# Optimization experiments

Hardware: AMD Instinct MI355X
Metric: run time of the kernel (lower is better)

Reference implementation:

```python
import jax, jax.numpy as jnp
import numpy as np

N_NODES = 8192
N_EDGES = 524288
IN_DIM = 256
HID1 = 128
HID2 = 64


def setup_inputs() -> dict:
    key = jax.random.key(0)
    ks = jax.random.split(key, 10)
    s = 0.05
    x = jax.random.normal(ks[0], (N_NODES, IN_DIM), dtype=jnp.float32)
    edge_index = jax.random.randint(ks[1], (2, N_EDGES), 0, N_NODES, dtype=jnp.int64)
    W1 = jax.random.normal(ks[2], (IN_DIM, HID1), dtype=jnp.float32) * s
    b1 = jnp.zeros((HID1,), dtype=jnp.float32)
    W2 = jax.random.normal(ks[3], (IN_DIM, HID1), dtype=jnp.float32) * s
    b2 = jnp.zeros((HID1,), dtype=jnp.float32)
    Wmu = jax.random.normal(ks[4], (2 * HID1, HID2), dtype=jnp.float32) * s
    bmu = jnp.zeros((HID2,), dtype=jnp.float32)
    Wlv = jax.random.normal(ks[5], (2 * HID1, HID2), dtype=jnp.float32) * s
    blv = jnp.zeros((HID2,), dtype=jnp.float32)
    return {"x": x, "edge_index": edge_index, "W1": W1, "b1": b1,
            "W2": W2, "b2": b2, "Wmu": Wmu, "bmu": bmu, "Wlv": Wlv, "blv": blv}


def _gcn(x, W, b, row, col, norm, n):
    # linear transform, edge-indexed gather, degree-normalized scale, scatter-add
    h = x @ W                                   # [N, out]
    msg = h[col] * norm[:, None]                # [E+N, out]
    agg = jax.ops.segment_sum(msg, row, num_segments=n)
    return agg + b


def reference(x, edge_index, W1, b1, W2, b2, Wmu, bmu, Wlv, blv):
    n = x.shape[0]
    loop = jnp.arange(n, dtype=edge_index.dtype)
    row = jnp.concatenate([edge_index[0], loop])   # add self-loops (GCNConv default)
    col = jnp.concatenate([edge_index[1], loop])
    deg = jax.ops.segment_sum(jnp.ones_like(row, dtype=x.dtype), row, num_segments=n)
    dinv = jnp.where(deg > 0, jax.lax.rsqrt(deg), 0.0)
    norm = dinv[row] * dinv[col]                   # symmetric D^-1/2 A_hat D^-1/2

    h1 = _gcn(x, W1, b1, row, col, norm, n)
    h2 = _gcn(x, W2, b2, row, col, norm, n)
    hc = jnp.concatenate([h1, h2], axis=1)         # [N, 2*HID1]
    mu = _gcn(hc, Wmu, bmu, row, col, norm, n)
    logvar = _gcn(hc, Wlv, blv, row, col, norm, n)
    z = mu                                         # eval-mode reparametrize -> mu
    adj = jax.nn.sigmoid(z @ z.T)                  # InnerProductDecoder.forward_all
    return adj, mu, logvar
```

## Files before the change

### kernel.cpp

```cpp
#include <hip/hip_runtime.h>
#include <hip/hip_bf16.h>

#define N_NODES 8192
#define N_EDGES 524288
#define TOT_EDGES (N_EDGES + N_NODES)
#define IN_DIM 256
#define HID1 128
#define HID2 64
#define DC 128
#define CAP 192
#define FILL_BLK 520

typedef __attribute__((ext_vector_type(8))) short bf16x8;
typedef __attribute__((ext_vector_type(4))) float f32x4;
typedef __attribute__((ext_vector_type(4))) int   i32x4;
typedef __attribute__((ext_vector_type(4))) unsigned short u16x4;

__device__ __forceinline__ float b2f(unsigned short u){
    unsigned int v = ((unsigned int)u) << 16;
    float f; __builtin_memcpy(&f, &v, 4); return f;
}
__device__ __forceinline__ unsigned short f2b(float f){
    __hip_bfloat16 h = __float2bfloat16(f);
    return *(unsigned short*)&h;
}


__global__ __launch_bounds__(256) void k_pre(const float* __restrict__ W1, const float* __restrict__ W2,
                                             const float* __restrict__ Wmu, const float* __restrict__ Wlv,
                                             const float* __restrict__ b1, const float* __restrict__ b2,
                                             unsigned short* __restrict__ WcT, float* __restrict__ cvec,
                                             float* __restrict__ zbase){
    int b = blockIdx.x, t = threadIdx.x;
    if (b < 8){
        ((f32x4*)zbase)[b*256 + t] = (f32x4){0.f,0.f,0.f,0.f};
    } else {
        int r = (b - 8)*2 + (t >> 7);
        int j = t & 127;
        const float* Wsel = (j < 64) ? Wmu : Wlv;
        int jj = j & 63;
        float acc = 0.f;
        for (int k=0;k<HID1;k++){
            acc += W1[r*HID1+k] * Wsel[k*HID2+jj] + W2[r*HID1+k] * Wsel[(HID1+k)*HID2+jj];
        }
        WcT[(size_t)j*IN_DIM + r] = f2b(acc);
        if (r == 0){
            float c = 0.f;
            for (int k=0;k<HID1;k++){
                c += b1[k]*Wsel[k*HID2+jj] + b2[k]*Wsel[(HID1+k)*HID2+jj];
            }
            cvec[j] = c;
        }
    }
}


__global__ __launch_bounds__(256) void k_fill_gemm(const int* __restrict__ ei, int* __restrict__ fillc,
                                                   unsigned short* __restrict__ slots,
                                                   const float* __restrict__ x,
                                                   const unsigned short* __restrict__ WcT,
                                                   unsigned short* __restrict__ Ubf){
    int b = blockIdx.x, t = threadIdx.x;
    if (b < FILL_BLK){
        int e4 = (b*256 + t)*4;
        if (e4 >= TOT_EDGES) return;
        if (e4 < N_EDGES){
            i32x4 rr = *(const i32x4*)(ei + e4);
            i32x4 cc = *(const i32x4*)(ei + N_EDGES + e4);
            #pragma unroll
            for (int j=0;j<4;j++){
                int s = atomicAdd(&fillc[rr[j]], 1);
                if (s < CAP) slots[(size_t)rr[j]*CAP + s] = (unsigned short)cc[j];
            }
        } else {
            #pragma unroll
            for (int j=0;j<4;j++){
                int r = e4 - N_EDGES + j;
                int s = atomicAdd(&fillc[r], 1);
                if (s < CAP) slots[(size_t)r*CAP + s] = (unsigned short)r;
            }
        }
    } else {
        int l  = t & 63;
        int w  = t >> 6;
        int Ibase = (b - FILL_BLK)*32;
        int Jbase = w*32;
        int lr = l & 15;
        int kg = l >> 4;
        f32x4 acc[2][2];
        #pragma unroll
        for (int mt=0;mt<2;mt++)
            #pragma unroll
            for (int nt=0;nt<2;nt++) acc[mt][nt] = (f32x4){0.f,0.f,0.f,0.f};
        #pragma unroll
        for (int kc=0; kc<IN_DIM/32; kc++){
            bf16x8 a[2], bb[2];
            #pragma unroll
            for (int mt=0;mt<2;mt++){
                const float* xr = x + (size_t)(Ibase+mt*16+lr)*IN_DIM + kc*32 + kg*8;
                f32x4 v0 = *(const f32x4*)xr;
                f32x4 v1 = *(const f32x4*)(xr + 4);
                #pragma unroll
                for (int j=0;j<4;j++){
                    a[mt][j]   = (short)f2b(v0[j]);
                    a[mt][4+j] = (short)f2b(v1[j]);
                }
            }
            #pragma unroll
            for (int nt=0;nt<2;nt++)
                bb[nt] = *(const bf16x8*)(WcT + (size_t)(Jbase+nt*16+lr)*IN_DIM + kc*32 + kg*8);
            #pragma unroll
            for (int mt=0;mt<2;mt++)
                #pragma unroll
                for (int nt=0;nt<2;nt++)
                    acc[mt][nt] = __builtin_amdgcn_mfma_f32_16x16x32_bf16(a[mt], bb[nt], acc[mt][nt], 0, 0, 0);
        }
        #pragma unroll
        for (int mt=0;mt<2;mt++)
            #pragma unroll
            for (int r=0;r<4;r++){
                int grow = Ibase + mt*16 + kg*4 + r;
                #pragma unroll
                for (int nt=0;nt<2;nt++)
                    Ubf[(size_t)grow*DC + Jbase + nt*16 + lr] = f2b(acc[mt][nt][r]);
            }
    }
}


__global__ __launch_bounds__(256) void k_spmm(const unsigned short* __restrict__ IN,
                                              const unsigned short* __restrict__ slots,
                                              const int* __restrict__ fillc,
                                              unsigned short* __restrict__ OUT){
    int tid = threadIdx.x;
    int i = blockIdx.x*4 + (tid >> 6);
    int l  = tid & 15;
    int eg = (tid >> 4) & 3;
    int deg = min(fillc[i], CAP);
    const unsigned short* sl = slots + (size_t)i*CAP;
    float acc[8] = {0.f,0.f,0.f,0.f,0.f,0.f,0.f,0.f};
    for (int e = eg; e < deg; e += 4){
        int c = sl[e];
        float wgt = rsqrtf((float)fillc[c]);
        bf16x8 v = *(const bf16x8*)(IN + (size_t)c*DC + l*8);
        #pragma unroll
        for (int j=0;j<8;j++) acc[j] += wgt * b2f((unsigned short)v[j]);
    }
    #pragma unroll
    for (int j=0;j<8;j++){
        acc[j] += __shfl_xor(acc[j], 16);
        acc[j] += __shfl_xor(acc[j], 32);
    }
    if (eg == 0){
        float di = rsqrtf((float)fillc[i]);
        bf16x8 o;
        #pragma unroll
        for (int j=0;j<8;j++) o[j] = (short)f2b(di*acc[j]);
        *(bf16x8*)(OUT + (size_t)i*DC + l*8) = o;
    }
}


__global__ __launch_bounds__(256) void k_spmm_out(const unsigned short* __restrict__ T,
                                                  const unsigned short* __restrict__ slots,
                                                  const int* __restrict__ fillc,
                                                  const float* __restrict__ cvec,
                                                  const float* __restrict__ bmu, const float* __restrict__ blv,
                                                  float* __restrict__ outMu, float* __restrict__ outLv,
                                                  unsigned short* __restrict__ muBf){
    int tid = threadIdx.x;
    int i = blockIdx.x*4 + (tid >> 6);
    int l  = tid & 15;
    int eg = (tid >> 4) & 3;
    int deg = min(fillc[i], CAP);
    const unsigned short* sl = slots + (size_t)i*CAP;
    float acc[8] = {0.f,0.f,0.f,0.f,0.f,0.f,0.f,0.f};
    float wsum = 0.f;
    for (int e = eg; e < deg; e += 4){
        int c = sl[e];
        float wgt = rsqrtf((float)fillc[c]);
        wsum += wgt;
        bf16x8 v = *(const bf16x8*)(T + (size_t)c*DC + l*8);
        #pragma unroll
        for (int j=0;j<8;j++) acc[j] += wgt * b2f((unsigned short)v[j]);
    }
    #pragma unroll
    for (int j=0;j<8;j++){
        acc[j] += __shfl_xor(acc[j], 16);
        acc[j] += __shfl_xor(acc[j], 32);
    }
    wsum += __shfl_xor(wsum, 16);
    wsum += __shfl_xor(wsum, 32);
    if (eg == 0){
        float di = rsqrtf((float)fillc[i]);
        float sv = di * wsum;
        float val[8];
        #pragma unroll
        for (int j=0;j<8;j++) val[j] = di*acc[j] + sv*cvec[l*8+j];
        if (l < 8){
            f32x4 v0, v1; bf16x8 o;
            #pragma unroll
            for (int j=0;j<8;j++){
                float vv = val[j] + bmu[l*8+j];
                if (j<4) v0[j] = vv; else v1[j-4] = vv;
                o[j] = (short)f2b(vv);
            }
            *(f32x4*)(outMu + (size_t)i*HID2 + l*8)     = v0;
            *(f32x4*)(outMu + (size_t)i*HID2 + l*8 + 4) = v1;
            *(bf16x8*)(muBf + (size_t)i*HID2 + l*8)     = o;
        } else {
            int d = (l-8)*8;
            f32x4 v0, v1;
            #pragma unroll
            for (int j=0;j<8;j++){
                float vv = val[j] + blv[d+j];
                if (j<4) v0[j] = vv; else v1[j-4] = vv;
            }
            *(f32x4*)(outLv + (size_t)i*HID2 + d)     = v0;
            *(f32x4*)(outLv + (size_t)i*HID2 + d + 4) = v1;
        }
    }
}


__global__ __launch_bounds__(256) void k_adj(const unsigned short* __restrict__ mu, float* __restrict__ adj){
    int t  = threadIdx.x;
    int l  = t & 63;
    int w  = t >> 6;
    int wr = w >> 1, wc = w & 1;
    int Ibase = blockIdx.y*128 + wr*64;
    int Jbase = blockIdx.x*128 + wc*64;
    int lr = l & 15;
    int kg = l >> 4;

    bf16x8 afr[4][2], bfr[4][2];
    #pragma unroll
    for (int mt=0; mt<4; mt++){
        const unsigned short* p = mu + (size_t)(Ibase + mt*16 + lr)*HID2 + kg*8;
        afr[mt][0] = *(const bf16x8*)(p);
        afr[mt][1] = *(const bf16x8*)(p + 32);
    }
    #pragma unroll
    for (int nt=0; nt<4; nt++){
        const unsigned short* p = mu + (size_t)(Jbase + nt*16 + lr)*HID2 + kg*8;
        bfr[nt][0] = *(const bf16x8*)(p);
        bfr[nt][1] = *(const bf16x8*)(p + 32);
    }

    f32x4 acc[4][4];
    #pragma unroll
    for (int mt=0; mt<4; mt++)
        #pragma unroll
        for (int nt=0; nt<4; nt++)
            acc[mt][nt] = (f32x4){0.f,0.f,0.f,0.f};

    #pragma unroll
    for (int kc=0; kc<2; kc++)
        #pragma unroll
        for (int mt=0; mt<4; mt++)
            #pragma unroll
            for (int nt=0; nt<4; nt++)
                acc[mt][nt] = __builtin_amdgcn_mfma_f32_16x16x32_bf16(afr[mt][kc], bfr[nt][kc], acc[mt][nt], 0, 0, 0);

    __shared__ float wt[4][16][68];
    float* myt = &wt[w][0][0];
    #pragma unroll
    for (int mt=0; mt<4; mt++){
        asm volatile("s_waitcnt lgkmcnt(0)" ::: "memory");
        #pragma unroll
        for (int nt=0; nt<4; nt++)
            #pragma unroll
            for (int r=0; r<4; r++)
                myt[(kg*4+r)*68 + nt*16 + lr] = acc[mt][nt][r];
        asm volatile("s_waitcnt lgkmcnt(0)" ::: "memory");
        __builtin_amdgcn_sched_barrier(0);
        #pragma unroll
        for (int p=0; p<4; p++){
            int row = p*4 + (l >> 4);
            int col = (l & 15)*4;
            f32x4 v = *(const f32x4*)&myt[row*68 + col];
            f32x4 o;
            #pragma unroll
            for (int j=0;j<4;j++)
                o[j] = __builtin_amdgcn_rcpf(1.f + __expf(-v[j]));
            *(f32x4*)(adj + (size_t)(Ibase + mt*16 + row)*N_NODES + Jbase + col) = o;
        }
    }
}


extern "C" void kernel_launch(void* const* d_in, const int* in_sizes, int n_in,
                              void* d_out, int out_size, void* d_ws, size_t ws_size,
                              hipStream_t stream){
    const float* x   = (const float*)d_in[0];
    const int*   ei  = (const int*)  d_in[1];
    const float* W1  = (const float*)d_in[2];
    const float* b1  = (const float*)d_in[3];
    const float* W2  = (const float*)d_in[4];
    const float* b2  = (const float*)d_in[5];
    const float* Wmu = (const float*)d_in[6];
    const float* bmu = (const float*)d_in[7];
    const float* Wlv = (const float*)d_in[8];
    const float* blv = (const float*)d_in[9];

    char* ws = (char*)d_ws;
    int*   fillc  = (int*)  (ws + 0);
    unsigned short* WcT = (unsigned short*)(ws + 32768);
    float* cvec   = (float*)(ws + 98304);
    unsigned short* muBf = (unsigned short*)(ws + 98816);

    float* adj   = (float*)d_out;
    float* outMu = adj + (size_t)N_NODES*N_NODES;
    float* outLv = outMu + (size_t)N_NODES*HID2;

    unsigned short* Ubf   = (unsigned short*)adj;
    unsigned short* Tbf   = (unsigned short*)((char*)adj + 16*1024*1024);
    unsigned short* slots = (unsigned short*)((char*)adj + 32*1024*1024);

    k_pre      <<<136, 256, 0, stream>>>(W1, W2, Wmu, Wlv, b1, b2, WcT, cvec, (float*)ws);
    k_fill_gemm<<<FILL_BLK + 256, 256, 0, stream>>>(ei, fillc, slots, x, WcT, Ubf);
    k_spmm     <<<N_NODES/4, 256, 0, stream>>>(Ubf, slots, fillc, Tbf);
    k_spmm_out <<<N_NODES/4, 256, 0, stream>>>(Tbf, slots, fillc, cvec, bmu, blv,
                                               outMu, outLv, muBf);
    k_adj      <<<dim3(N_NODES/128, N_NODES/128), 256, 0, stream>>>(muBf, adj);
}
```

Baseline: 128.5 us.

## Retile adjacency decoder so each wave writes full 1KB contiguous row segments

```diff
diff --git a/kernel.cpp b/kernel.cpp
--- a/kernel.cpp
+++ b/kernel.cpp
@@ -227,63 +227,54 @@
     int t  = threadIdx.x;
     int l  = t & 63;
     int w  = t >> 6;
-    int wr = w >> 1, wc = w & 1;
-    int Ibase = blockIdx.y*128 + wr*64;
-    int Jbase = blockIdx.x*128 + wc*64;
     int lr = l & 15;
     int kg = l >> 4;
-
-    bf16x8 afr[4][2], bfr[4][2];
-    #pragma unroll
-    for (int mt=0; mt<4; mt++){
-        const unsigned short* p = mu + (size_t)(Ibase + mt*16 + lr)*HID2 + kg*8;
-        afr[mt][0] = *(const bf16x8*)(p);
-        afr[mt][1] = *(const bf16x8*)(p + 32);
-    }
-    #pragma unroll
-    for (int nt=0; nt<4; nt++){
-        const unsigned short* p = mu + (size_t)(Jbase + nt*16 + lr)*HID2 + kg*8;
-        bfr[nt][0] = *(const bf16x8*)(p);
-        bfr[nt][1] = *(const bf16x8*)(p + 32);
-    }
-
-    f32x4 acc[4][4];
-    #pragma unroll
-    for (int mt=0; mt<4; mt++)
-        #pragma unroll
-        for (int nt=0; nt<4; nt++)
-            acc[mt][nt] = (f32x4){0.f,0.f,0.f,0.f};
-
-    #pragma unroll
-    for (int kc=0; kc<2; kc++)
-        #pragma unroll
-        for (int mt=0; mt<4; mt++)
-            #pragma unroll
-            for (int nt=0; nt<4; nt++)
-                acc[mt][nt] = __builtin_amdgcn_mfma_f32_16x16x32_bf16(afr[mt][kc], bfr[nt][kc], acc[mt][nt], 0, 0, 0);
-
-    __shared__ float wt[4][16][68];
+    int Rbase = blockIdx.y*64 + w*16;
+    int Cbase = blockIdx.x*256;
+
+    bf16x8 afr[2];
+    {
+        const unsigned short* pa = mu + (size_t)(Rbase + lr)*HID2 + kg*8;
+        afr[0] = *(const bf16x8*)(pa);
+        afr[1] = *(const bf16x8*)(pa + 32);
+    }
+
+    f32x4 acc[16];
+    #pragma unroll
+    for (int nt=0; nt<16; nt++) acc[nt] = (f32x4){0.f,0.f,0.f,0.f};
+
+    #pragma unroll
+    for (int nt=0; nt<16; nt++){
+        const unsigned short* pb = mu + (size_t)(Cbase + nt*16 + lr)*HID2 + kg*8;
+        bf16x8 b0 = *(const bf16x8*)(pb);
+        bf16x8 b1 = *(const bf16x8*)(pb + 32);
+        acc[nt] = __builtin_amdgcn_mfma_f32_16x16x32_bf16(afr[0], b0, acc[nt], 0, 0, 0);
+        acc[nt] = __builtin_amdgcn_mfma_f32_16x16x32_bf16(afr[1], b1, acc[nt], 0, 0, 0);
+    }
+
+    __shared__ float wt[4][8][260];
     float* myt = &wt[w][0][0];
-    #pragma unroll
-    for (int mt=0; mt<4; mt++){
-        asm volatile("s_waitcnt lgkmcnt(0)" ::: "memory");
-        #pragma unroll
-        for (int nt=0; nt<4; nt++)
-            #pragma unroll
-            for (int r=0; r<4; r++)
-                myt[(kg*4+r)*68 + nt*16 + lr] = acc[mt][nt][r];
+
+    #pragma unroll
+    for (int ph=0; ph<2; ph++){
+        if ((kg >> 1) == ph){
+            int rloc = (kg & 1)*4;
+            #pragma unroll
+            for (int nt=0; nt<16; nt++)
+                #pragma unroll
+                for (int r=0; r<4; r++)
+                    myt[(rloc + r)*260 + nt*16 + lr] = acc[nt][r];
+        }
         asm volatile("s_waitcnt lgkmcnt(0)" ::: "memory");
         __builtin_amdgcn_sched_barrier(0);
         #pragma unroll
-        for (int p=0; p<4; p++){
-            int row = p*4 + (l >> 4);
-            int col = (l & 15)*4;
-            f32x4 v = *(const f32x4*)&myt[row*68 + col];
+        for (int p=0; p<8; p++){
+            f32x4 v = *(const f32x4*)&myt[p*260 + l*4];
             f32x4 o;
             #pragma unroll
             for (int j=0;j<4;j++)
                 o[j] = __builtin_amdgcn_rcpf(1.f + __expf(-v[j]));
-            *(f32x4*)(adj + (size_t)(Ibase + mt*16 + row)*N_NODES + Jbase + col) = o;
+            *(f32x4*)(adj + (size_t)(Rbase + ph*8 + p)*N_NODES + Cbase + l*4) = o;
         }
     }
 }
@@ -322,5 +313,5 @@
     k_spmm     <<<N_NODES/4, 256, 0, stream>>>(Ubf, slots, fillc, Tbf);
     k_spmm_out <<<N_NODES/4, 256, 0, stream>>>(Tbf, slots, fillc, cvec, bmu, blv,
                                                outMu, outLv, muBf);
-    k_adj      <<<dim3(N_NODES/128, N_NODES/128), 256, 0, stream>>>(muBf, adj);
-}
+    k_adj      <<<dim3(N_NODES/256, N_NODES/64), 256, 0, stream>>>(muBf, adj);
+}
```

Measured after the change: 167.1 us. 1.3x slower.
